# Optimization experiments

Measured on AMD Instinct MI355X. Metric: run time of the kernel, lower is better.

## Reference

```python
import jax, jax.numpy as jnp
import numpy as np

R_CUT = 10.0
ROUNDS = 1  # num_message_passing_rounds


def setup_inputs() -> dict:
    key = jax.random.key(0)
    N, DEG, S, NRBF, G = 10000, 16, 128, 20, 64
    E = N * DEG
    ks = jax.random.split(key, 16)
    w = lambda k, shp, fan: (jax.random.normal(k, shp, dtype=jnp.float32) / np.float32(np.sqrt(fan)))
    return {
        "edge_vector_diffs": jax.random.normal(ks[0], (E, 3), dtype=jnp.float32) * 3.0,
        "edge_lengths": jax.random.uniform(ks[1], (E,), dtype=jnp.float32) * 15.0,
        "node_from": jnp.repeat(jnp.arange(N), DEG),            # every node has DEG outgoing edges
        "node_graph_index": jax.random.randint(ks[2], (N,), 0, G),
        "num_graphs": G,
        "emb0": jax.random.normal(ks[3], (S,), dtype=jnp.float32) * 0.01,  # embedding.weight[0]
        "phi_w1": w(ks[4], (S, S), S), "phi_b1": jnp.zeros((S,), jnp.float32),
        "phi_w2": w(ks[5], (S, 3 * S), S), "phi_b2": jnp.zeros((3 * S,), jnp.float32),
        "filt_w": w(ks[6], (NRBF, 3 * S), NRBF), "filt_b": jnp.zeros((3 * S,), jnp.float32),
        "u_w": w(ks[7], (S, S), S), "v_w": w(ks[8], (S, S), S),
        "upd_w1": w(ks[9], (2 * S, S), 2 * S), "upd_b1": jnp.zeros((S,), jnp.float32),
        "upd_w2": w(ks[10], (S, 3 * S), S), "upd_b2": jnp.zeros((3 * S,), jnp.float32),
        "out_w1": w(ks[11], (S, S), S), "out_b1": jnp.zeros((S,), jnp.float32),
        "out_w2": w(ks[12], (S, 1), S), "out_b2": jnp.zeros((1,), jnp.float32),
    }


def reference(edge_vector_diffs, edge_lengths, node_from, node_graph_index, num_graphs,
              emb0, phi_w1, phi_b1, phi_w2, phi_b2, filt_w, filt_b, u_w, v_w,
              upd_w1, upd_b1, upd_w2, upd_b2, out_w1, out_b1, out_w2, out_b2):
    S = phi_w1.shape[0]
    N = node_graph_index.shape[0]
    NRBF = filt_w.shape[0]
    silu = jax.nn.silu
    seg = lambda v, n: jax.ops.segment_sum(v, node_from, num_segments=n)

    mask = (jnp.abs(edge_lengths) <= R_CUT).astype(jnp.float32)          # [E] nbr_mask
    r = jnp.linalg.norm(edge_vector_diffs, axis=1)                        # [E]
    r_safe = jnp.maximum(r, 1e-12)
    k = jnp.arange(1, NRBF + 1, dtype=jnp.float32)
    # PAINN sinc radial basis sin(k*pi*r/r_cut)/r, then linear -> [E, 3S]
    rbf = jnp.sin(k[None, :] * jnp.pi * r_safe[:, None] / R_CUT) / r_safe[:, None]
    cutoff = 0.5 * (jnp.cos(jnp.pi * r / R_CUT) + 1.0) * (r < R_CUT)      # cosine cutoff
    W = (rbf @ filt_w + filt_b) * cutoff[:, None]                          # [E, 3S]

    tile3 = jnp.arange(S) % 3  # xyzxyz... truncation pattern from .repeat(...)[: S]
    # scalar Frobenius norm of each node's masked neighbor-diff block
    frob = jnp.sqrt(seg(mask * r * r, N))                                  # [N]
    denom_e = frob[node_from]
    denom_e = jnp.where(denom_e > 0, denom_e, 1.0)
    normalized = edge_vector_diffs / denom_e[:, None]                      # [E, 3]
    norm_exp = normalized[:, tile3]                                        # [E, S]

    # state init: sum over dim 1 of embedding(zeros) == S * embedding.weight[0]
    state = jnp.broadcast_to(jnp.float32(S) * emb0, (N, S))
    state_vec = jnp.zeros((N, 3, S), jnp.float32)

    for _ in range(ROUNDS):
        # message block (nbrs_node_from == destination node, so sync update == original sequential loop)
        phi = silu(state[node_from] @ phi_w1 + phi_b1) @ phi_w2 + phi_b2   # [E, 3S]
        prod = phi * W
        m1, m2, m3 = prod[:, :S], prod[:, S:2 * S], prod[:, 2 * S:]
        vec_msg = state_vec[node_from] * m1[:, None, :] + (norm_exp * m3)[:, None, :]  # [E,3,S]
        state = seg(m2 * mask[:, None], N)                                 # [N, S]
        state_vec = seg(vec_msg * mask[:, None, None], N)                  # [N, 3, S]
        # update block
        U = jnp.einsum('nps,st->npt', state_vec, u_w)                      # [N,3,S]
        V = jnp.einsum('nps,st->npt', state_vec, v_w)
        UV = jnp.einsum('nps,nqs->npq', U, V)                              # [N,3,3]
        Vnorm = jnp.sqrt(jnp.sum(V * V, axis=1))                           # [N,S]
        a = silu(jnp.concatenate([Vnorm, state], axis=-1) @ upd_w1 + upd_b1) @ upd_w2 + upd_b2
        a_vv, a_sv, a_ss = a[:, :S], a[:, S:2 * S], a[:, 2 * S:]
        uv_tiled = jnp.sum(UV, axis=1)[:, tile3]                           # [N,S]
        state = a_ss + uv_tiled * a_sv
        state_vec = U * a_vv[:, None, :]

    graph_state = jax.ops.segment_sum(state, node_graph_index, num_segments=num_graphs)
    out = (silu(graph_state @ out_w1 + out_b1) @ out_w2 + out_b2).ravel()  # [num_graphs]
    return out
```

## Files before the change

### kernel.cpp

```cpp
#include <hip/hip_runtime.h>
#include <math.h>

#define NN   10000
#define DEG  16
#define SS   128
#define NRBF 20
#define GG   64
#define RC   10.0f
#define PI_F 3.14159265358979323846f
#define NB   8

__device__ __forceinline__ float silu_f(float x){
    return x / (1.0f + __expf(-x));
}

__global__ __launch_bounds__(128) void k_phi(
    const float* __restrict__ emb0,
    const float* __restrict__ w1, const float* __restrict__ b1,
    const float* __restrict__ w2, const float* __restrict__ b2,
    float* __restrict__ phiW, float* __restrict__ gs){
    __shared__ float s0[SS];
    __shared__ float hL[SS];
    int t = threadIdx.x;
    for (int i = t; i < GG*SS; i += 128) gs[i] = 0.0f;
    s0[t] = 128.0f * emb0[t];
    __syncthreads();
    float acc = b1[t];
    for (int s = 0; s < SS; s++) acc = fmaf(s0[s], w1[s*SS + t], acc);
    hL[t] = silu_f(acc);
    __syncthreads();
    for (int c = t; c < 3*SS; c += 128){
        float a = b2[c];
        for (int j = 0; j < SS; j++) a = fmaf(hL[j], w2[j*3*SS + c], a);
        phiW[c] = a;
    }
}

__global__ __launch_bounds__(256) void k_edge(
    const float* __restrict__ evd, const float* __restrict__ elen,
    const int* __restrict__ node_from,
    const float* __restrict__ filt_w, const float* __restrict__ filt_b,
    const float* __restrict__ phiW,
    float* __restrict__ state, float* __restrict__ sv){
    __shared__ float rS[DEG];
    __shared__ float mcL[DEG];
    __shared__ float frL[DEG];
    __shared__ float eV[DEG][3];
    __shared__ float rbfL[DEG][NRBF];
    __shared__ float invD;
    int n = blockIdx.x;
    int t = threadIdx.x;

    if (t < DEG){
        int e = n*DEG + t;
        float x = evd[3*e+0], y = evd[3*e+1], z = evd[3*e+2];
        float r = sqrtf(x*x + y*y + z*z);
        float len  = elen[e];
        float mask = (fabsf(len) <= RC) ? 1.0f : 0.0f;
        float cut  = (r < RC) ? 0.5f*(cosf(PI_F*r*(1.0f/RC)) + 1.0f) : 0.0f;
        rS[t]  = fmaxf(r, 1e-12f);
        mcL[t] = mask * cut;
        frL[t] = mask * r * r;
        eV[t][0] = x; eV[t][1] = y; eV[t][2] = z;
    }
    __syncthreads();
    for (int idx = t; idx < DEG*NRBF; idx += 256){
        int e = idx / NRBF, k = idx % NRBF;
        float rs = rS[e];
        rbfL[e][k] = sinf((float)(k+1) * (PI_F/RC) * rs) / rs;
    }
    if (t == 0){
        float s = 0.0f;
        for (int e = 0; e < DEG; e++) s += frL[e];
        float fb = sqrtf(s);
        invD = (fb > 0.0f) ? 1.0f/fb : 1.0f;
    }
    __syncthreads();

    int c  = t;
    int gc = SS + c;
    float fw[NRBF];
    #pragma unroll
    for (int k = 0; k < NRBF; k++) fw[k] = filt_w[k*(3*SS) + gc];
    float fb  = filt_b[gc];
    float ph  = phiW[gc];
    float iD  = invD;
    int   s3  = (c >= SS) ? ((c - SS) % 3) : 0;

    float acc = 0.0f;
    for (int e = 0; e < DEG; e++){
        float mc = mcL[e];
        if (mc == 0.0f) continue;
        const float4* rv = (const float4*)(&rbfL[e][0]);
        float4 r0 = rv[0], r1 = rv[1], r2 = rv[2], r3 = rv[3], r4 = rv[4];
        float w = fb;
        w = fmaf(r0.x, fw[0],  w); w = fmaf(r0.y, fw[1],  w);
        w = fmaf(r0.z, fw[2],  w); w = fmaf(r0.w, fw[3],  w);
        w = fmaf(r1.x, fw[4],  w); w = fmaf(r1.y, fw[5],  w);
        w = fmaf(r1.z, fw[6],  w); w = fmaf(r1.w, fw[7],  w);
        w = fmaf(r2.x, fw[8],  w); w = fmaf(r2.y, fw[9],  w);
        w = fmaf(r2.z, fw[10], w); w = fmaf(r2.w, fw[11], w);
        w = fmaf(r3.x, fw[12], w); w = fmaf(r3.y, fw[13], w);
        w = fmaf(r3.z, fw[14], w); w = fmaf(r3.w, fw[15], w);
        w = fmaf(r4.x, fw[16], w); w = fmaf(r4.y, fw[17], w);
        w = fmaf(r4.z, fw[18], w); w = fmaf(r4.w, fw[19], w);
        float v   = ph * mc * w;
        float fac = (c < SS) ? 1.0f : eV[e][s3] * iD;
        acc = fmaf(v, fac, acc);
    }
    int nf = node_from[n*DEG];
    if (c < SS) state[nf*SS + c]        = acc;
    else        sv[nf*SS + (c - SS)]    = acc;
}

__global__ __launch_bounds__(128) void k_update(
    const float* __restrict__ state, const float* __restrict__ sv,
    const float* __restrict__ u_w, const float* __restrict__ v_w,
    const float* __restrict__ upd_w1, const float* __restrict__ upd_b1,
    const float* __restrict__ upd_w2, const float* __restrict__ upd_b2,
    const int* __restrict__ ngi, float* __restrict__ gs){
    __shared__ float svT[SS][NB];
    __shared__ float xT[2*SS][NB];
    __shared__ float h2T[SS][NB];
    __shared__ float red[2][NB];
    __shared__ float dL[NB];
    int t  = threadIdx.x;
    int n0 = blockIdx.x * NB;

    for (int idx = t; idx < NB*SS; idx += 128){
        int b = idx >> 7, s = idx & (SS-1);
        svT[s][b]     = sv[(n0+b)*SS + s];
        xT[SS+s][b]   = state[(n0+b)*SS + s];
    }
    __syncthreads();

    float accU[NB], accV[NB];
    #pragma unroll
    for (int b = 0; b < NB; b++){ accU[b]=0.f; accV[b]=0.f; }
    for (int s = 0; s < SS; s++){
        float wu = u_w[s*SS + t];
        float wv = v_w[s*SS + t];
        const float4* sp = (const float4*)(&svT[s][0]);
        float4 s03 = sp[0], s47 = sp[1];
        float svv[NB] = {s03.x,s03.y,s03.z,s03.w,s47.x,s47.y,s47.z,s47.w};
        #pragma unroll
        for (int b = 0; b < NB; b++){
            accU[b] = fmaf(svv[b], wu, accU[b]);
            accV[b] = fmaf(svv[b], wv, accV[b]);
        }
    }

    int lane = t & 63, wid = t >> 6;
    #pragma unroll
    for (int b = 0; b < NB; b++){
        float p = accU[b]*accV[b];
        for (int off = 32; off; off >>= 1) p += __shfl_down(p, off);
        if (lane == 0) red[wid][b] = p;
    }
    {
        float4 q0, q1;
        q0.x = sqrtf(3.f*accV[0]*accV[0]); q0.y = sqrtf(3.f*accV[1]*accV[1]);
        q0.z = sqrtf(3.f*accV[2]*accV[2]); q0.w = sqrtf(3.f*accV[3]*accV[3]);
        q1.x = sqrtf(3.f*accV[4]*accV[4]); q1.y = sqrtf(3.f*accV[5]*accV[5]);
        q1.z = sqrtf(3.f*accV[6]*accV[6]); q1.w = sqrtf(3.f*accV[7]*accV[7]);
        ((float4*)(&xT[t][0]))[0] = q0;
        ((float4*)(&xT[t][0]))[1] = q1;
    }
    __syncthreads();
    if (t < NB) dL[t] = red[0][t] + red[1][t];

    float accH[NB];
    #pragma unroll
    for (int b = 0; b < NB; b++) accH[b] = 0.f;
    for (int i = 0; i < 2*SS; i++){
        float w = upd_w1[i*SS + t];
        const float4* xp = (const float4*)(&xT[i][0]);
        float4 x03 = xp[0], x47 = xp[1];
        float xv[NB] = {x03.x,x03.y,x03.z,x03.w,x47.x,x47.y,x47.z,x47.w};
        #pragma unroll
        for (int b = 0; b < NB; b++) accH[b] = fmaf(xv[b], w, accH[b]);
    }
    float b1v = upd_b1[t];
    {
        float4 q0, q1;
        q0.x = silu_f(accH[0]+b1v); q0.y = silu_f(accH[1]+b1v);
        q0.z = silu_f(accH[2]+b1v); q0.w = silu_f(accH[3]+b1v);
        q1.x = silu_f(accH[4]+b1v); q1.y = silu_f(accH[5]+b1v);
        q1.z = silu_f(accH[6]+b1v); q1.w = silu_f(accH[7]+b1v);
        ((float4*)(&h2T[t][0]))[0] = q0;
        ((float4*)(&h2T[t][0]))[1] = q1;
    }
    __syncthreads();

    float a1[NB], a2[NB];
    #pragma unroll
    for (int b = 0; b < NB; b++){ a1[b]=0.f; a2[b]=0.f; }
    for (int j = 0; j < SS; j++){
        float w1 = upd_w2[j*3*SS + SS   + t];
        float w2 = upd_w2[j*3*SS + 2*SS + t];
        const float4* hp = (const float4*)(&h2T[j][0]);
        float4 h03 = hp[0], h47 = hp[1];
        float hv[NB] = {h03.x,h03.y,h03.z,h03.w,h47.x,h47.y,h47.z,h47.w};
        #pragma unroll
        for (int b = 0; b < NB; b++){
            a1[b] = fmaf(hv[b], w1, a1[b]);
            a2[b] = fmaf(hv[b], w2, a2[b]);
        }
    }
    float bsv = upd_b2[SS+t], bss = upd_b2[2*SS+t];
    #pragma unroll
    for (int b = 0; b < NB; b++){
        float ns = (a2[b] + bss) + 3.0f*dL[b]*(a1[b] + bsv);
        int g = ngi[n0+b];
        atomicAdd(&gs[g*SS + t], ns);
    }
}

__global__ __launch_bounds__(128) void k_out(
    const float* __restrict__ gs,
    const float* __restrict__ w1, const float* __restrict__ b1,
    const float* __restrict__ w2, const float* __restrict__ b2,
    float* __restrict__ out){
    __shared__ float gsL[SS];
    __shared__ float red[2];
    int g = blockIdx.x, t = threadIdx.x;
    gsL[t] = gs[g*SS + t];
    __syncthreads();
    float acc = b1[t];
    for (int s = 0; s < SS; s++) acc = fmaf(gsL[s], w1[s*SS + t], acc);
    float p = silu_f(acc) * w2[t];
    for (int off = 32; off; off >>= 1) p += __shfl_down(p, off);
    if ((t & 63) == 0) red[t >> 6] = p;
    __syncthreads();
    if (t == 0) out[g] = red[0] + red[1] + b2[0];
}

extern "C" void kernel_launch(void* const* d_in, const int* in_sizes, int n_in,
                              void* d_out, int out_size, void* d_ws, size_t ws_size,
                              hipStream_t stream) {
    const float* evd     = (const float*)d_in[0];
    const float* elen    = (const float*)d_in[1];
    const int*   nfrom   = (const int*)  d_in[2];
    const int*   ngi     = (const int*)  d_in[3];
    const float* emb0    = (const float*)d_in[5];
    const float* phi_w1  = (const float*)d_in[6];
    const float* phi_b1  = (const float*)d_in[7];
    const float* phi_w2  = (const float*)d_in[8];
    const float* phi_b2  = (const float*)d_in[9];
    const float* filt_w  = (const float*)d_in[10];
    const float* filt_b  = (const float*)d_in[11];
    const float* u_w     = (const float*)d_in[12];
    const float* v_w     = (const float*)d_in[13];
    const float* upd_w1  = (const float*)d_in[14];
    const float* upd_b1  = (const float*)d_in[15];
    const float* upd_w2  = (const float*)d_in[16];
    const float* upd_b2  = (const float*)d_in[17];
    const float* out_w1  = (const float*)d_in[18];
    const float* out_b1  = (const float*)d_in[19];
    const float* out_w2  = (const float*)d_in[20];
    const float* out_b2  = (const float*)d_in[21];

    float* ws    = (float*)d_ws;
    float* phiW  = ws;
    float* state = ws + 512;
    float* sv    = state + NN*SS;
    float* gs    = sv + NN*SS;

    k_phi<<<1, 128, 0, stream>>>(emb0, phi_w1, phi_b1, phi_w2, phi_b2, phiW, gs);
    k_edge<<<NN, 256, 0, stream>>>(evd, elen, nfrom, filt_w, filt_b, phiW, state, sv);
    k_update<<<NN/NB, 128, 0, stream>>>(state, sv, u_w, v_w,
                                        upd_w1, upd_b1, upd_w2, upd_b2, ngi, gs);
    k_out<<<GG, 128, 0, stream>>>(gs, out_w1, out_b1, out_w2, out_b2, (float*)d_out);
}
```

Measured before the change: 193.7 us.

## Halve edge-kernel threads and retile update GEMMs with swizzled shared layout

The edge kernel now runs 128 threads per node, and each thread computes both the state and vector channel, so the shared RBF loads are reused across two filter columns. The update kernel changes its thread mapping so each thread owns one node and 8 contiguous output columns. Weights are loaded as float4 vectors, and activations are kept in an XOR-swizzled shared layout to avoid bank conflicts. The intent is to cut weight reload traffic and shared-memory conflicts. The cost is higher register pressure and 8 atomics per thread, which now target contiguous columns.

```diff
diff --git a/kernel.cpp b/kernel.cpp
--- a/kernel.cpp
+++ b/kernel.cpp
@@ -12,6 +12,10 @@
 
 __device__ __forceinline__ float silu_f(float x){
     return x / (1.0f + __expf(-x));
+}
+
+__device__ __forceinline__ int lidx(int i, int b){
+    return (i << 3) | ((b ^ i) & 7);
 }
 
 __global__ __launch_bounds__(128) void k_phi(
@@ -36,7 +40,7 @@
     }
 }
 
-__global__ __launch_bounds__(256) void k_edge(
+__global__ __launch_bounds__(128) void k_edge(
     const float* __restrict__ evd, const float* __restrict__ elen,
     const int* __restrict__ node_from,
     const float* __restrict__ filt_w, const float* __restrict__ filt_b,
@@ -64,7 +68,7 @@
         eV[t][0] = x; eV[t][1] = y; eV[t][2] = z;
     }
     __syncthreads();
-    for (int idx = t; idx < DEG*NRBF; idx += 256){
+    for (int idx = t; idx < DEG*NRBF; idx += 128){
         int e = idx / NRBF, k = idx % NRBF;
         float rs = rS[e];
         rbfL[e][k] = sinf((float)(k+1) * (PI_F/RC) * rs) / rs;
@@ -72,45 +76,45 @@
     if (t == 0){
         float s = 0.0f;
         for (int e = 0; e < DEG; e++) s += frL[e];
-        float fb = sqrtf(s);
-        invD = (fb > 0.0f) ? 1.0f/fb : 1.0f;
-    }
-    __syncthreads();
-
-    int c  = t;
-    int gc = SS + c;
-    float fw[NRBF];
-    #pragma unroll
-    for (int k = 0; k < NRBF; k++) fw[k] = filt_w[k*(3*SS) + gc];
-    float fb  = filt_b[gc];
-    float ph  = phiW[gc];
+        float fbn = sqrtf(s);
+        invD = (fbn > 0.0f) ? 1.0f/fbn : 1.0f;
+    }
+    __syncthreads();
+
+    int gc1 = SS + t;
+    int gc2 = 2*SS + t;
+    float fw1[NRBF], fw2[NRBF];
+    #pragma unroll
+    for (int k = 0; k < NRBF; k++){
+        fw1[k] = filt_w[k*(3*SS) + gc1];
+        fw2[k] = filt_w[k*(3*SS) + gc2];
+    }
+    float fb1 = filt_b[gc1], fb2 = filt_b[gc2];
+    float ph1 = phiW[gc1],   ph2 = phiW[gc2];
     float iD  = invD;
-    int   s3  = (c >= SS) ? ((c - SS) % 3) : 0;
-
-    float acc = 0.0f;
+    int   s3  = t % 3;
+
+    float acc1 = 0.0f, acc2 = 0.0f;
     for (int e = 0; e < DEG; e++){
         float mc = mcL[e];
         if (mc == 0.0f) continue;
         const float4* rv = (const float4*)(&rbfL[e][0]);
         float4 r0 = rv[0], r1 = rv[1], r2 = rv[2], r3 = rv[3], r4 = rv[4];
-        float w = fb;
-        w = fmaf(r0.x, fw[0],  w); w = fmaf(r0.y, fw[1],  w);
-        w = fmaf(r0.z, fw[2],  w); w = fmaf(r0.w, fw[3],  w);
-        w = fmaf(r1.x, fw[4],  w); w = fmaf(r1.y, fw[5],  w);
-        w = fmaf(r1.z, fw[6],  w); w = fmaf(r1.w, fw[7],  w);
-        w = fmaf(r2.x, fw[8],  w); w = fmaf(r2.y, fw[9],  w);
-        w = fmaf(r2.z, fw[10], w); w = fmaf(r2.w, fw[11], w);
-        w = fmaf(r3.x, fw[12], w); w = fmaf(r3.y, fw[13], w);
-        w = fmaf(r3.z, fw[14], w); w = fmaf(r3.w, fw[15], w);
-        w = fmaf(r4.x, fw[16], w); w = fmaf(r4.y, fw[17], w);
-        w = fmaf(r4.z, fw[18], w); w = fmaf(r4.w, fw[19], w);
-        float v   = ph * mc * w;
-        float fac = (c < SS) ? 1.0f : eV[e][s3] * iD;
-        acc = fmaf(v, fac, acc);
+        float rr[20] = {r0.x,r0.y,r0.z,r0.w, r1.x,r1.y,r1.z,r1.w,
+                        r2.x,r2.y,r2.z,r2.w, r3.x,r3.y,r3.z,r3.w,
+                        r4.x,r4.y,r4.z,r4.w};
+        float w1 = fb1, w2 = fb2;
+        #pragma unroll
+        for (int k = 0; k < NRBF; k++){
+            w1 = fmaf(rr[k], fw1[k], w1);
+            w2 = fmaf(rr[k], fw2[k], w2);
+        }
+        acc1 = fmaf(ph1*mc, w1, acc1);
+        acc2 = fmaf(ph2*mc*eV[e][s3]*iD, w2, acc2);
     }
     int nf = node_from[n*DEG];
-    if (c < SS) state[nf*SS + c]        = acc;
-    else        sv[nf*SS + (c - SS)]    = acc;
+    state[nf*SS + t] = acc1;
+    sv[nf*SS + t]    = acc2;
 }
 
 __global__ __launch_bounds__(128) void k_update(
@@ -119,100 +123,105 @@
     const float* __restrict__ upd_w1, const float* __restrict__ upd_b1,
     const float* __restrict__ upd_w2, const float* __restrict__ upd_b2,
     const int* __restrict__ ngi, float* __restrict__ gs){
-    __shared__ float svT[SS][NB];
-    __shared__ float xT[2*SS][NB];
-    __shared__ float h2T[SS][NB];
-    __shared__ float red[2][NB];
+    __shared__ float svT[SS*NB];
+    __shared__ float xT[2*SS*NB];
+    __shared__ float red[2*NB];
     __shared__ float dL[NB];
+    __shared__ int   gIdx[NB];
     int t  = threadIdx.x;
+    int b  = t & 7, q = t >> 3, c0 = q*8;
     int n0 = blockIdx.x * NB;
 
+    if (t < NB) gIdx[t] = ngi[n0 + t];
     for (int idx = t; idx < NB*SS; idx += 128){
-        int b = idx >> 7, s = idx & (SS-1);
-        svT[s][b]     = sv[(n0+b)*SS + s];
-        xT[SS+s][b]   = state[(n0+b)*SS + s];
-    }
-    __syncthreads();
-
-    float accU[NB], accV[NB];
-    #pragma unroll
-    for (int b = 0; b < NB; b++){ accU[b]=0.f; accV[b]=0.f; }
-    for (int s = 0; s < SS; s++){
-        float wu = u_w[s*SS + t];
-        float wv = v_w[s*SS + t];
-        const float4* sp = (const float4*)(&svT[s][0]);
-        float4 s03 = sp[0], s47 = sp[1];
-        float svv[NB] = {s03.x,s03.y,s03.z,s03.w,s47.x,s47.y,s47.z,s47.w};
-        #pragma unroll
-        for (int b = 0; b < NB; b++){
-            accU[b] = fmaf(svv[b], wu, accU[b]);
-            accV[b] = fmaf(svv[b], wv, accV[b]);
+        int bb = idx >> 7, s = idx & (SS-1);
+        svT[lidx(s, bb)]      = sv[(n0+bb)*SS + s];
+        xT[lidx(SS+s, bb)]    = state[(n0+bb)*SS + s];
+    }
+    __syncthreads();
+
+    float accU[8], accV[8];
+    #pragma unroll
+    for (int k = 0; k < 8; k++){ accU[k] = 0.f; accV[k] = 0.f; }
+    #pragma unroll 4
+    for (int i = 0; i < SS; i++){
+        float xv = svT[lidx(i, b)];
+        float wu[8], wv[8];
+        *(float4*)&wu[0] = *(const float4*)(u_w + i*SS + c0);
+        *(float4*)&wu[4] = *(const float4*)(u_w + i*SS + c0 + 4);
+        *(float4*)&wv[0] = *(const float4*)(v_w + i*SS + c0);
+        *(float4*)&wv[4] = *(const float4*)(v_w + i*SS + c0 + 4);
+        #pragma unroll
+        for (int k = 0; k < 8; k++){
+            accU[k] = fmaf(xv, wu[k], accU[k]);
+            accV[k] = fmaf(xv, wv[k], accV[k]);
         }
     }
 
-    int lane = t & 63, wid = t >> 6;
-    #pragma unroll
-    for (int b = 0; b < NB; b++){
-        float p = accU[b]*accV[b];
-        for (int off = 32; off; off >>= 1) p += __shfl_down(p, off);
-        if (lane == 0) red[wid][b] = p;
+    float pd = 0.f;
+    #pragma unroll
+    for (int k = 0; k < 8; k++) pd = fmaf(accU[k], accV[k], pd);
+    pd += __shfl_xor(pd, 8);
+    pd += __shfl_xor(pd, 16);
+    pd += __shfl_xor(pd, 32);
+    if ((t & 63) < NB) red[(t >> 6)*NB + b] = pd;
+
+    const float SQ3 = 1.7320508075688772f;
+    #pragma unroll
+    for (int k = 0; k < 8; k++) xT[lidx(c0+k, b)] = SQ3 * fabsf(accV[k]);
+    __syncthreads();
+    if (t < NB) dL[t] = red[t] + red[NB + t];
+
+    float accH[8];
+    #pragma unroll
+    for (int k = 0; k < 8; k++) accH[k] = 0.f;
+    #pragma unroll 4
+    for (int i = 0; i < 2*SS; i++){
+        float xv = xT[lidx(i, b)];
+        float w[8];
+        *(float4*)&w[0] = *(const float4*)(upd_w1 + i*SS + c0);
+        *(float4*)&w[4] = *(const float4*)(upd_w1 + i*SS + c0 + 4);
+        #pragma unroll
+        for (int k = 0; k < 8; k++) accH[k] = fmaf(xv, w[k], accH[k]);
     }
     {
-        float4 q0, q1;
-        q0.x = sqrtf(3.f*accV[0]*accV[0]); q0.y = sqrtf(3.f*accV[1]*accV[1]);
-        q0.z = sqrtf(3.f*accV[2]*accV[2]); q0.w = sqrtf(3.f*accV[3]*accV[3]);
-        q1.x = sqrtf(3.f*accV[4]*accV[4]); q1.y = sqrtf(3.f*accV[5]*accV[5]);
-        q1.z = sqrtf(3.f*accV[6]*accV[6]); q1.w = sqrtf(3.f*accV[7]*accV[7]);
-        ((float4*)(&xT[t][0]))[0] = q0;
-        ((float4*)(&xT[t][0]))[1] = q1;
-    }
-    __syncthreads();
-    if (t < NB) dL[t] = red[0][t] + red[1][t];
-
-    float accH[NB];
-    #pragma unroll
-    for (int b = 0; b < NB; b++) accH[b] = 0.f;
-    for (int i = 0; i < 2*SS; i++){
-        float w = upd_w1[i*SS + t];
-        const float4* xp = (const float4*)(&xT[i][0]);
-        float4 x03 = xp[0], x47 = xp[1];
-        float xv[NB] = {x03.x,x03.y,x03.z,x03.w,x47.x,x47.y,x47.z,x47.w};
-        #pragma unroll
-        for (int b = 0; b < NB; b++) accH[b] = fmaf(xv[b], w, accH[b]);
-    }
-    float b1v = upd_b1[t];
-    {
-        float4 q0, q1;
-        q0.x = silu_f(accH[0]+b1v); q0.y = silu_f(accH[1]+b1v);
-        q0.z = silu_f(accH[2]+b1v); q0.w = silu_f(accH[3]+b1v);
-        q1.x = silu_f(accH[4]+b1v); q1.y = silu_f(accH[5]+b1v);
-        q1.z = silu_f(accH[6]+b1v); q1.w = silu_f(accH[7]+b1v);
-        ((float4*)(&h2T[t][0]))[0] = q0;
-        ((float4*)(&h2T[t][0]))[1] = q1;
-    }
-    __syncthreads();
-
-    float a1[NB], a2[NB];
-    #pragma unroll
-    for (int b = 0; b < NB; b++){ a1[b]=0.f; a2[b]=0.f; }
+        float bb1[8];
+        *(float4*)&bb1[0] = *(const float4*)(upd_b1 + c0);
+        *(float4*)&bb1[4] = *(const float4*)(upd_b1 + c0 + 4);
+        #pragma unroll
+        for (int k = 0; k < 8; k++)
+            svT[lidx(c0+k, b)] = silu_f(accH[k] + bb1[k]);
+    }
+    __syncthreads();
+
+    float a2[8], a3[8];
+    #pragma unroll
+    for (int k = 0; k < 8; k++){ a2[k] = 0.f; a3[k] = 0.f; }
+    #pragma unroll 4
     for (int j = 0; j < SS; j++){
-        float w1 = upd_w2[j*3*SS + SS   + t];
-        float w2 = upd_w2[j*3*SS + 2*SS + t];
-        const float4* hp = (const float4*)(&h2T[j][0]);
-        float4 h03 = hp[0], h47 = hp[1];
-        float hv[NB] = {h03.x,h03.y,h03.z,h03.w,h47.x,h47.y,h47.z,h47.w};
-        #pragma unroll
-        for (int b = 0; b < NB; b++){
-            a1[b] = fmaf(hv[b], w1, a1[b]);
-            a2[b] = fmaf(hv[b], w2, a2[b]);
+        float hx = svT[lidx(j, b)];
+        float w2a[8], w3a[8];
+        *(float4*)&w2a[0] = *(const float4*)(upd_w2 + j*3*SS + SS + c0);
+        *(float4*)&w2a[4] = *(const float4*)(upd_w2 + j*3*SS + SS + c0 + 4);
+        *(float4*)&w3a[0] = *(const float4*)(upd_w2 + j*3*SS + 2*SS + c0);
+        *(float4*)&w3a[4] = *(const float4*)(upd_w2 + j*3*SS + 2*SS + c0 + 4);
+        #pragma unroll
+        for (int k = 0; k < 8; k++){
+            a2[k] = fmaf(hx, w2a[k], a2[k]);
+            a3[k] = fmaf(hx, w3a[k], a3[k]);
         }
     }
-    float bsv = upd_b2[SS+t], bss = upd_b2[2*SS+t];
-    #pragma unroll
-    for (int b = 0; b < NB; b++){
-        float ns = (a2[b] + bss) + 3.0f*dL[b]*(a1[b] + bsv);
-        int g = ngi[n0+b];
-        atomicAdd(&gs[g*SS + t], ns);
+    float dlb = dL[b];
+    int   g   = gIdx[b];
+    float bsv[8], bss[8];
+    *(float4*)&bsv[0] = *(const float4*)(upd_b2 + SS   + c0);
+    *(float4*)&bsv[4] = *(const float4*)(upd_b2 + SS   + c0 + 4);
+    *(float4*)&bss[0] = *(const float4*)(upd_b2 + 2*SS + c0);
+    *(float4*)&bss[4] = *(const float4*)(upd_b2 + 2*SS + c0 + 4);
+    #pragma unroll
+    for (int k = 0; k < 8; k++){
+        float ns = (a3[k] + bss[k]) + 3.0f*dlb*(a2[k] + bsv[k]);
+        atomicAdd(&gs[g*SS + c0 + k], ns);
     }
 }
 
@@ -267,7 +276,7 @@
     float* gs    = sv + NN*SS;
 
     k_phi<<<1, 128, 0, stream>>>(emb0, phi_w1, phi_b1, phi_w2, phi_b2, phiW, gs);
-    k_edge<<<NN, 256, 0, stream>>>(evd, elen, nfrom, filt_w, filt_b, phiW, state, sv);
+    k_edge<<<NN, 128, 0, stream>>>(evd, elen, nfrom, filt_w, filt_b, phiW, state, sv);
     k_update<<<NN/NB, 128, 0, stream>>>(state, sv, u_w, v_w,
                                         upd_w1, upd_b1, upd_w2, upd_b2, ngi, gs);
     k_out<<<GG, 128, 0, stream>>>(gs, out_w1, out_b1, out_w2, out_b2, (float*)d_out);
```

Result: slower. 298.6 us (+54.2%).
